# Performance work log

Measured on AMD Instinct MI355X. Metric: run time of the kernel, lower is better.

The kernel has to match this reference:

```python
import jax, jax.numpy as jnp
import numpy as np

B = 16384   # batch (agents x parallel envs)
IN = 12     # input_dim
H = 64      # hidden_dim -> 2H = 128
OUT = 25    # output_dim (forced by x[:,0:5]..x[:,20:25] slicing)


def setup_inputs() -> dict:
    key = jax.random.key(0)
    ks = jax.random.split(key, 24)
    n = lambda k, s: jax.random.normal(k, s, dtype=jnp.float32)
    s = 0.1  # scale params to keep SiLU/softmax in a sane range
    return {
        "x": n(ks[0], (B, IN)),
        "na": 4,
        # mlp_in: Linear(IN, 2H) + SiLU
        "W_in": n(ks[1], (2 * H, IN)) * s, "b_in": n(ks[2], (2 * H,)) * s,
        # first attention (2H)
        "Aq4": n(ks[3], (2 * H, 2 * H)) * s, "Bq4": n(ks[4], (2 * H,)) * s,
        "Ak4": n(ks[5], (2 * H, 2 * H)) * s, "Bk4": n(ks[6], (2 * H,)) * s,
        "Av4": n(ks[7], (2 * H, 2 * H)) * s, "Bv4": n(ks[8], (2 * H,)) * s,
        # mlp_hidden_4: Linear(2H, H) + SiLU
        "W_h": n(ks[9], (H, 2 * H)) * s, "b_h": n(ks[10], (H,)) * s,
        # second attention (H)
        "Aq7": n(ks[11], (H, H)) * s, "Bq7": n(ks[12], (H,)) * s,
        "Ak7": n(ks[13], (H, H)) * s, "Bk7": n(ks[14], (H,)) * s,
        "Av7": n(ks[15], (H, H)) * s, "Bv7": n(ks[16], (H,)) * s,
        # mlp_out: Linear(H, OUT) + SiLU
        "W_out": n(ks[17], (OUT, H)) * s, "b_out": n(ks[18], (OUT,)) * s,
    }


def _attn(h, Aq, Bq, Ak, Bk, Av, Bv):
    # h: [B, D]; torch does bmm(A, x^T)+B with x of shape [B,1,D] -> seq-len-1
    # attention, i.e. scores are an outer product q k^T of shape [B, D, D].
    q = jax.nn.silu(h @ Aq.T + Bq)                      # [B, D]
    k = jax.nn.silu(h @ Ak.T + Bk)                      # [B, D]
    v = jax.nn.silu(h @ Av.T + Bv)                      # [B, D]
    a = jax.nn.softmax(q[:, :, None] * k[:, None, :], axis=2)  # [B, D, D]
    return jax.nn.silu(jnp.einsum("bij,bj->bi", a, v))  # [B, D]


def reference(x, na, W_in, b_in, Aq4, Bq4, Ak4, Bk4, Av4, Bv4,
              W_h, b_h, Aq7, Bq7, Ak7, Bk7, Av7, Bv7, W_out, b_out):
    h = jax.nn.silu(x @ W_in.T + b_in)                  # [B, 2H]
    h = _attn(h, Aq4, Bq4, Ak4, Bk4, Av4, Bv4)          # [B, 2H]
    h = jax.nn.silu(h @ W_h.T + b_h)                    # [B, H]
    h = _attn(h, Aq7, Bq7, Ak7, Bk7, Av7, Bv7)          # [B, H]
    y = jax.nn.silu(h @ W_out.T + b_out)                # [B, 25]

    # block-diagonal quadratic-form assembly (l=2, kron with ones(1,2))
    M11 = jnp.sum(y[:, 0:5] ** 2, axis=1)               # [B]
    M12 = jnp.sum(y[:, 5:10] ** 2, axis=1)
    M21 = jnp.sum(y[:, 10:15] ** 2, axis=1)
    M22 = jnp.sum(y[:, 15:20] ** 2, axis=1)
    Mpp = jnp.sum(y[:, 20:25] ** 2, axis=1)             # [B]
    q = y[:, :4]                                        # [B, 4] = [q0,q1,q2,q3]
    # M = [[diag(M11), diag(M12)],[diag(M21), diag(M22)]] (each 2x2 diag)
    quad = (M11 * (q[:, 0] ** 2 + q[:, 1] ** 2)
            + (M12 + M21) * (q[:, 0] * q[:, 2] + q[:, 1] * q[:, 3])
            + M22 * (q[:, 2] ** 2 + q[:, 3] ** 2))
    return (quad + Mpp)[:, None]                        # [B, 1]
```

## Files before the change

kernel.cpp:

```cpp
#include <hip/hip_runtime.h>

#define RPW 4
#define WAVES 4
#define RPB (RPW * WAVES)
#define NM 14

using short8 = __attribute__((ext_vector_type(8))) short;
using f32x4  = __attribute__((ext_vector_type(4))) float;

#define LOG2E 1.4426950408889634f

static __device__ __forceinline__ float ex2(float x) { return __builtin_amdgcn_exp2f(x); }
static __device__ __forceinline__ float rcpf_(float x) { return __builtin_amdgcn_rcpf(x); }
static __device__ __forceinline__ float silu_(float x) {
    return x * rcpf_(1.0f + ex2(-x * LOG2E));
}
static __device__ __forceinline__ unsigned short bfhi(float x) {
    return (unsigned short)(__float_as_uint(x) >> 16);
}
static __device__ __forceinline__ unsigned short bfrn(float x) {
    unsigned u = __float_as_uint(x);
    return (unsigned short)((u + 0x7fffu + ((u >> 16) & 1u)) >> 16);
}
static __device__ __forceinline__ float bf2f(unsigned short h) {
    return __uint_as_float(((unsigned)h) << 16);
}

template <int CTRL>
static __device__ __forceinline__ float dpp_rot(float v) {
    return __uint_as_float(
        __builtin_amdgcn_update_dpp(0u, __float_as_uint(v), CTRL, 0xF, 0xF, true));
}
static __device__ __forceinline__ float rsum16(float v) {
    v += dpp_rot<0x128>(v);
    v += dpp_rot<0x124>(v);
    v += dpp_rot<0x122>(v);
    v += dpp_rot<0x121>(v);
    return v;
}

__constant__ float c_invfact[15] = {
    1.f, 1.f, 0.5f, 1.f/6, 1.f/24, 1.f/120, 1.f/720, 1.f/5040, 1.f/40320,
    1.f/362880, 1.f/3628800, 1.f/39916800, 1.f/479001600,
    1.f/6227020800.f, 1.f/87178291200.f};

template <int O, int I>
__device__ __forceinline__ void tr(const float* __restrict__ s, float* __restrict__ d,
                                   int t0, int stride) {
    for (int idx = t0; idx < O * I; idx += stride) {
        int o = idx / I, in = idx - o * I;
        d[in * O + o] = s[idx];
    }
}
template <int N>
__device__ __forceinline__ void cvt(const float* __restrict__ s,
                                    unsigned short* __restrict__ hi,
                                    unsigned short* __restrict__ lo,
                                    int t0, int stride) {
    for (int i = t0; i < N; i += stride) {
        float a = s[i];
        unsigned short h = bfhi(a);
        float r = a - bf2f(h);
        hi[i] = h;
        lo[i] = bfhi(r);
    }
}

__global__ void tweights(const float* __restrict__ s0, const float* __restrict__ s1,
                         const float* __restrict__ s2, const float* __restrict__ s3,
                         const float* __restrict__ s4, const float* __restrict__ s5,
                         const float* __restrict__ s6, const float* __restrict__ s7,
                         const float* __restrict__ s8, float* __restrict__ ws) {
    const int stride = gridDim.x * blockDim.x;
    const int t0 = blockIdx.x * blockDim.x + threadIdx.x;
    tr<128, 12>(s0, ws + 0, t0, stride);
    unsigned short* u4 = (unsigned short*)(ws + 1536);
    cvt<128 * 128>(s1, u4 + 0,     u4 + 16384, t0, stride);
    cvt<128 * 128>(s2, u4 + 32768, u4 + 49152, t0, stride);
    cvt<128 * 128>(s3, u4 + 65536, u4 + 81920, t0, stride);
    unsigned short* wh = (unsigned short*)(ws + 50688);
    cvt<64 * 128>(s4, wh + 0, wh + 8192, t0, stride);
    unsigned short* u7 = (unsigned short*)(ws + 58880);
    cvt<64 * 64>(s5, u7 + 0,     u7 + 4096,  t0, stride);
    cvt<64 * 64>(s6, u7 + 8192,  u7 + 12288, t0, stride);
    cvt<64 * 64>(s7, u7 + 16384, u7 + 20480, t0, stride);
    tr<25, 64>(s8, ws + 71168, t0, stride);
}

__global__ __launch_bounds__(256, 4) void fused_net(
    const float* __restrict__ x, const float* __restrict__ ws,
    const float* __restrict__ b_in,
    const float* __restrict__ Bq4, const float* __restrict__ Bk4, const float* __restrict__ Bv4,
    const float* __restrict__ b_h,
    const float* __restrict__ Bq7, const float* __restrict__ Bk7, const float* __restrict__ Bv7,
    const float* __restrict__ b_out,
    float* __restrict__ out) {
    __shared__ __align__(16) unsigned short hAhi[16][136], hAlo[16][136];
    __shared__ __align__(16) unsigned short h2hi[16][80],  h2lo[16][80];
    __shared__ __align__(16) float sQ[16][132];
    __shared__ __align__(16) unsigned short sKVb[16][132][2];
    __shared__ __align__(16) float h3T[WAVES][64][RPW];
    __shared__ __align__(16) float sXT[WAVES][12][RPW];
    __shared__ __align__(16) float sY[WAVES][RPW][26];

    const int tid = threadIdx.x;
    const int w = tid >> 6;
    const int l = tid & 63;
    const int row0 = blockIdx.x * RPB + w * RPW;
    const int m16 = l & 15, quad = l >> 4;
    const int g = l & 15, r = l >> 4;
    const int R = w * RPW + r;

    const float* WinT  = ws + 0;
    const float* WoutT = ws + 71168;

    if (l < 12 * RPW) {
        float v = x[row0 * 12 + l];
        int rr = l / 12, in = l - rr * 12;
        sXT[w][in][rr] = v;
    }

    {
        float2 bb = *(const float2*)&b_in[2 * l];
        float a0[RPW], a1[RPW];
        #pragma unroll
        for (int rr = 0; rr < RPW; rr++) { a0[rr] = bb.x; a1[rr] = bb.y; }
        #pragma unroll
        for (int in = 0; in < 12; in++) {
            float2 wv = *(const float2*)&WinT[in * 128 + 2 * l];
            float4 xr = *(const float4*)&sXT[w][in][0];
            a0[0] = fmaf(xr.x, wv.x, a0[0]); a1[0] = fmaf(xr.x, wv.y, a1[0]);
            a0[1] = fmaf(xr.y, wv.x, a0[1]); a1[1] = fmaf(xr.y, wv.y, a1[1]);
            a0[2] = fmaf(xr.z, wv.x, a0[2]); a1[2] = fmaf(xr.z, wv.y, a1[2]);
            a0[3] = fmaf(xr.w, wv.x, a0[3]); a1[3] = fmaf(xr.w, wv.y, a1[3]);
        }
        #pragma unroll
        for (int rr = 0; rr < RPW; rr++) {
            float h0 = silu_(a0[rr]), h1 = silu_(a1[rr]);
            unsigned short h0h = bfhi(h0), h1h = bfhi(h1);
            float r0 = h0 - bf2f(h0h), r1 = h1 - bf2f(h1h);
            *(unsigned*)&hAhi[w * 4 + rr][2 * l] = (unsigned)h0h | ((unsigned)h1h << 16);
            *(unsigned*)&hAlo[w * 4 + rr][2 * l] = (unsigned)bfhi(r0) | ((unsigned)bfhi(r1) << 16);
        }
    }
    __syncthreads();

    {
        short8 Ah[4], Al[4];
        #pragma unroll
        for (int kt = 0; kt < 4; kt++) {
            Ah[kt] = *(const short8*)&hAhi[m16][kt * 32 + quad * 8];
            Al[kt] = *(const short8*)&hAlo[m16][kt * 32 + quad * 8];
        }
        const unsigned short* u4 = (const unsigned short*)(ws + 1536);
        #pragma unroll
        for (int t = 0; t < 6; t++) {
            const int nt = w * 6 + t;
            const int mat = nt >> 3;
            const int n = (nt & 7) * 16 + m16;
            const float* bp = (mat == 0) ? Bq4 : (mat == 1) ? Bk4 : Bv4;
            float b = bp[n];
            f32x4 acc = {b, b, b, b};
            const unsigned short* Bh = u4 + mat * 32768 + n * 128;
            const unsigned short* Bl = Bh + 16384;
            #pragma unroll
            for (int kt = 0; kt < 4; kt++) {
                short8 bh = *(const short8*)&Bh[kt * 32 + quad * 8];
                short8 bl = *(const short8*)&Bl[kt * 32 + quad * 8];
                acc = __builtin_amdgcn_mfma_f32_16x16x32_bf16(Ah[kt], bh, acc, 0, 0, 0);
                acc = __builtin_amdgcn_mfma_f32_16x16x32_bf16(Ah[kt], bl, acc, 0, 0, 0);
                acc = __builtin_amdgcn_mfma_f32_16x16x32_bf16(Al[kt], bh, acc, 0, 0, 0);
            }
            #pragma unroll
            for (int reg = 0; reg < 4; reg++) {
                int row = quad * 4 + reg;
                float val = silu_(acc[reg]);
                if (mat == 0)      sQ[row][n] = val;
                else if (mat == 1) sKVb[row][n][0] = bfrn(val);
                else               sKVb[row][n][1] = bfrn(val);
            }
        }
    }
    __syncthreads();

    {
        float dmom[NM];
        float nmom[NM + 1];
        #pragma unroll
        for (int m = 0; m < NM; m++) dmom[m] = 0.f;
        #pragma unroll
        for (int m = 0; m <= NM; m++) nmom[m] = 0.f;
        uint4 u0 = *(const uint4*)&sKVb[R][g * 8][0];
        uint4 u1 = *(const uint4*)&sKVb[R][g * 8 + 4][0];
        unsigned us[8] = {u0.x, u0.y, u0.z, u0.w, u1.x, u1.y, u1.z, u1.w};
        #pragma unroll
        for (int jj = 0; jj < 8; jj++) {
            unsigned u = us[jj];
            float kf = __uint_as_float(u << 16);
            float vf = __uint_as_float(u & 0xffff0000u);
            nmom[0] += vf;
            float p = kf;
            dmom[0] += p; nmom[1] = fmaf(vf, p, nmom[1]);
            #pragma unroll
            for (int m = 1; m < NM; m++) {
                p *= kf;
                dmom[m] += p;
                nmom[m + 1] = fmaf(vf, p, nmom[m + 1]);
            }
        }
        #pragma unroll
        for (int m = 0; m < NM; m++) dmom[m] = rsum16(dmom[m]);
        #pragma unroll
        for (int m = 0; m <= NM; m++) nmom[m] = rsum16(nmom[m]);
        float cd[NM + 1], cn[NM + 1];
        cd[0] = 128.f; cn[0] = nmom[0];
        #pragma unroll
        for (int m = 1; m <= NM; m++) {
            cd[m] = dmom[m - 1] * c_invfact[m];
            cn[m] = nmom[m] * c_invfact[m];
        }
        float4 qa = *(const float4*)&sQ[R][g * 8];
        float4 qb = *(const float4*)&sQ[R][g * 8 + 4];
        float qs[8] = {qa.x, qa.y, qa.z, qa.w, qb.x, qb.y, qb.z, qb.w};
        unsigned hiw[4], low[4];
        #pragma unroll
        for (int i = 0; i < 8; i++) {
            float t = qs[i];
            float d = cd[NM], nn = cn[NM];
            #pragma unroll
            for (int m = NM - 1; m >= 0; m--) {
                d = fmaf(d, t, cd[m]);
                nn = fmaf(nn, t, cn[m]);
            }
            float o = silu_(nn * rcpf_(d));
            unsigned short oh = bfhi(o);
            unsigned short olo = bfhi(o - bf2f(oh));
            if (i & 1) { hiw[i >> 1] |= ((unsigned)oh) << 16; low[i >> 1] |= ((unsigned)olo) << 16; }
            else       { hiw[i >> 1] = oh; low[i >> 1] = olo; }
        }
        *(uint4*)&hAhi[R][g * 8] = make_uint4(hiw[0], hiw[1], hiw[2], hiw[3]);
        *(uint4*)&hAlo[R][g * 8] = make_uint4(low[0], low[1], low[2], low[3]);
    }
    __syncthreads();

    {
        short8 Ah[4], Al[4];
        #pragma unroll
        for (int kt = 0; kt < 4; kt++) {
            Ah[kt] = *(const short8*)&hAhi[m16][kt * 32 + quad * 8];
            Al[kt] = *(const short8*)&hAlo[m16][kt * 32 + quad * 8];
        }
        const unsigned short* whh = (const unsigned short*)(ws + 50688);
        const unsigned short* whl = whh + 8192;
        const int n = w * 16 + m16;
        float b = b_h[n];
        f32x4 acc = {b, b, b, b};
        #pragma unroll
        for (int kt = 0; kt < 4; kt++) {
            short8 bh = *(const short8*)&whh[n * 128 + kt * 32 + quad * 8];
            short8 bl = *(const short8*)&whl[n * 128 + kt * 32 + quad * 8];
            acc = __builtin_amdgcn_mfma_f32_16x16x32_bf16(Ah[kt], bh, acc, 0, 0, 0);
            acc = __builtin_amdgcn_mfma_f32_16x16x32_bf16(Ah[kt], bl, acc, 0, 0, 0);
            acc = __builtin_amdgcn_mfma_f32_16x16x32_bf16(Al[kt], bh, acc, 0, 0, 0);
        }
        #pragma unroll
        for (int reg = 0; reg < 4; reg++) {
            int row = quad * 4 + reg;
            float hv = silu_(acc[reg]);
            unsigned short hh = bfhi(hv);
            h2hi[row][n] = hh;
            h2lo[row][n] = bfhi(hv - bf2f(hh));
        }
    }
    __syncthreads();

    {
        short8 Ah[2], Al[2];
        #pragma unroll
        for (int kt = 0; kt < 2; kt++) {
            Ah[kt] = *(const short8*)&h2hi[m16][kt * 32 + quad * 8];
            Al[kt] = *(const short8*)&h2lo[m16][kt * 32 + quad * 8];
        }
        const unsigned short* u7 = (const unsigned short*)(ws + 58880);
        #pragma unroll
        for (int t = 0; t < 3; t++) {
            const int nt = w * 3 + t;
            const int mat = nt >> 2;
            const int n = (nt & 3) * 16 + m16;
            const float* bp = (mat == 0) ? Bq7 : (mat == 1) ? Bk7 : Bv7;
            float b = bp[n];
            f32x4 acc = {b, b, b, b};
            const unsigned short* Bh = u7 + mat * 8192 + n * 64;
            const unsigned short* Bl = Bh + 4096;
            #pragma unroll
            for (int kt = 0; kt < 2; kt++) {
                short8 bh = *(const short8*)&Bh[kt * 32 + quad * 8];
                short8 bl = *(const short8*)&Bl[kt * 32 + quad * 8];
                acc = __builtin_amdgcn_mfma_f32_16x16x32_bf16(Ah[kt], bh, acc, 0, 0, 0);
                acc = __builtin_amdgcn_mfma_f32_16x16x32_bf16(Ah[kt], bl, acc, 0, 0, 0);
                acc = __builtin_amdgcn_mfma_f32_16x16x32_bf16(Al[kt], bh, acc, 0, 0, 0);
            }
            #pragma unroll
            for (int reg = 0; reg < 4; reg++) {
                int row = quad * 4 + reg;
                float val = silu_(acc[reg]);
                if (mat == 0)      sQ[row][n] = val;
                else if (mat == 1) sKVb[row][n][0] = bfrn(val);
                else               sKVb[row][n][1] = bfrn(val);
            }
        }
    }
    __syncthreads();

    {
        float dmom[NM];
        float nmom[NM + 1];
        #pragma unroll
        for (int m = 0; m < NM; m++) dmom[m] = 0.f;
        #pragma unroll
        for (int m = 0; m <= NM; m++) nmom[m] = 0.f;
        uint4 u0 = *(const uint4*)&sKVb[R][g * 4][0];
        unsigned us[4] = {u0.x, u0.y, u0.z, u0.w};
        #pragma unroll
        for (int jj = 0; jj < 4; jj++) {
            unsigned u = us[jj];
            float kf = __uint_as_float(u << 16);
            float vf = __uint_as_float(u & 0xffff0000u);
            nmom[0] += vf;
            float p = kf;
            dmom[0] += p; nmom[1] = fmaf(vf, p, nmom[1]);
            #pragma unroll
            for (int m = 1; m < NM; m++) {
                p *= kf;
                dmom[m] += p;
                nmom[m + 1] = fmaf(vf, p, nmom[m + 1]);
            }
        }
        #pragma unroll
        for (int m = 0; m < NM; m++) dmom[m] = rsum16(dmom[m]);
        #pragma unroll
        for (int m = 0; m <= NM; m++) nmom[m] = rsum16(nmom[m]);
        float cd[NM + 1], cn[NM + 1];
        cd[0] = 64.f; cn[0] = nmom[0];
        #pragma unroll
        for (int m = 1; m <= NM; m++) {
            cd[m] = dmom[m - 1] * c_invfact[m];
            cn[m] = nmom[m] * c_invfact[m];
        }
        float4 qa = *(const float4*)&sQ[R][g * 4];
        float qs[4] = {qa.x, qa.y, qa.z, qa.w};
        #pragma unroll
        for (int i = 0; i < 4; i++) {
            float t = qs[i];
            float d = cd[NM], nn = cn[NM];
            #pragma unroll
            for (int m = NM - 1; m >= 0; m--) {
                d = fmaf(d, t, cd[m]);
                nn = fmaf(nn, t, cn[m]);
            }
            h3T[w][g * 4 + i][r] = silu_(nn * rcpf_(d));
        }
    }

    {
        const int o = l & 31;
        const int half = l >> 5;
        const int oc = (o < 25) ? o : 0;
        float y[RPW];
        float bb = (half == 0) ? b_out[oc] : 0.f;
        #pragma unroll
        for (int rr = 0; rr < RPW; rr++) y[rr] = bb;
        const int in0 = half * 32;
        #pragma unroll 4
        for (int i = 0; i < 32; i++) {
            int in = in0 + i;
            float wv = WoutT[in * 25 + oc];
            float4 xr = *(const float4*)&h3T[w][in][0];
            y[0] = fmaf(xr.x, wv, y[0]);
            y[1] = fmaf(xr.y, wv, y[1]);
            y[2] = fmaf(xr.z, wv, y[2]);
            y[3] = fmaf(xr.w, wv, y[3]);
        }
        #pragma unroll
        for (int rr = 0; rr < RPW; rr++) {
            float full = y[rr] + __shfl_xor(y[rr], 32, 64);
            if (l < 25) sY[w][rr][l] = silu_(full);
        }
    }

    if (l < RPW) {
        const int rr = l;
        float y[25];
        #pragma unroll
        for (int c = 0; c < 25; c++) y[c] = sY[w][rr][c];
        float M11 = 0.f, M12 = 0.f, M21 = 0.f, M22 = 0.f, Mpp = 0.f;
        #pragma unroll
        for (int c = 0; c < 5; c++) {
            M11 = fmaf(y[c], y[c], M11);
            M12 = fmaf(y[5 + c], y[5 + c], M12);
            M21 = fmaf(y[10 + c], y[10 + c], M21);
            M22 = fmaf(y[15 + c], y[15 + c], M22);
            Mpp = fmaf(y[20 + c], y[20 + c], Mpp);
        }
        float quad = M11 * (y[0] * y[0] + y[1] * y[1])
                   + (M12 + M21) * (y[0] * y[2] + y[1] * y[3])
                   + M22 * (y[2] * y[2] + y[3] * y[3]);
        out[row0 + rr] = quad + Mpp;
    }
}

extern "C" void kernel_launch(void* const* d_in, const int* in_sizes, int n_in,
                              void* d_out, int out_size, void* d_ws, size_t ws_size,
                              hipStream_t stream) {
    const float* x    = (const float*)d_in[0];
    const float* W_in = (const float*)d_in[2];
    const float* b_in = (const float*)d_in[3];
    const float* Aq4  = (const float*)d_in[4];
    const float* Bq4  = (const float*)d_in[5];
    const float* Ak4  = (const float*)d_in[6];
    const float* Bk4  = (const float*)d_in[7];
    const float* Av4  = (const float*)d_in[8];
    const float* Bv4  = (const float*)d_in[9];
    const float* W_h  = (const float*)d_in[10];
    const float* b_h  = (const float*)d_in[11];
    const float* Aq7  = (const float*)d_in[12];
    const float* Bq7  = (const float*)d_in[13];
    const float* Ak7  = (const float*)d_in[14];
    const float* Bk7  = (const float*)d_in[15];
    const float* Av7  = (const float*)d_in[16];
    const float* Bv7  = (const float*)d_in[17];
    const float* Wout = (const float*)d_in[18];
    const float* bout = (const float*)d_in[19];
    float* ws = (float*)d_ws;

    tweights<<<256, 256, 0, stream>>>(W_in, Aq4, Ak4, Av4, W_h, Aq7, Ak7, Av7, Wout, ws);

    const int B = in_sizes[0] / 12;
    const int grid = B / RPB;
    fused_net<<<grid, 256, 0, stream>>>(x, ws, b_in, Bq4, Bk4, Bv4,
                                        b_h, Bq7, Bk7, Bv7, bout, (float*)d_out);
}
```

Before: 137.1 us.

## Halve rows per wave and spread attention moments across 32 lanes

Reduces rows per wave from 4 to 2 (8 rows per block), so each row's attention moment computation is spread over 32 lanes instead of 16. Each lane now handles half as many keys and queries, and a ds_swizzle step extends the DPP reduction to 32 lanes. MFMA tiles still compute 16 rows but only the first 8 are valid, which wastes half of the matrix-core work, and the grid doubles in size. Launch bounds are raised to 8 blocks per CU to gain occupancy, at the risk of register pressure.

```diff
diff --git a/kernel.cpp b/kernel.cpp
--- a/kernel.cpp
+++ b/kernel.cpp
@@ -1,6 +1,6 @@
 #include <hip/hip_runtime.h>
 
-#define RPW 4
+#define RPW 2
 #define WAVES 4
 #define RPB (RPW * WAVES)
 #define NM 14
@@ -36,6 +36,12 @@
     v += dpp_rot<0x124>(v);
     v += dpp_rot<0x122>(v);
     v += dpp_rot<0x121>(v);
+    return v;
+}
+static __device__ __forceinline__ float rsum32(float v) {
+    v = rsum16(v);
+    v += __uint_as_float(
+        (unsigned)__builtin_amdgcn_ds_swizzle((int)__float_as_uint(v), 0x401F));
     return v;
 }
 
@@ -87,7 +93,7 @@
     tr<25, 64>(s8, ws + 71168, t0, stride);
 }
 
-__global__ __launch_bounds__(256, 4) void fused_net(
+__global__ __launch_bounds__(256, 8) void fused_net(
     const float* __restrict__ x, const float* __restrict__ ws,
     const float* __restrict__ b_in,
     const float* __restrict__ Bq4, const float* __restrict__ Bk4, const float* __restrict__ Bv4,
@@ -95,10 +101,10 @@
     const float* __restrict__ Bq7, const float* __restrict__ Bk7, const float* __restrict__ Bv7,
     const float* __restrict__ b_out,
     float* __restrict__ out) {
-    __shared__ __align__(16) unsigned short hAhi[16][136], hAlo[16][136];
-    __shared__ __align__(16) unsigned short h2hi[16][80],  h2lo[16][80];
-    __shared__ __align__(16) float sQ[16][132];
-    __shared__ __align__(16) unsigned short sKVb[16][132][2];
+    __shared__ __align__(16) unsigned short hAhi[8][136], hAlo[8][136];
+    __shared__ __align__(16) unsigned short h2hi[8][80],  h2lo[8][80];
+    __shared__ __align__(16) float sQ[8][132];
+    __shared__ __align__(16) unsigned short sKVb[8][132][2];
     __shared__ __align__(16) float h3T[WAVES][64][RPW];
     __shared__ __align__(16) float sXT[WAVES][12][RPW];
     __shared__ __align__(16) float sY[WAVES][RPW][26];
@@ -108,7 +114,8 @@
     const int l = tid & 63;
     const int row0 = blockIdx.x * RPB + w * RPW;
     const int m16 = l & 15, quad = l >> 4;
-    const int g = l & 15, r = l >> 4;
+    const int m8 = m16 & 7;
+    const int g = l & 31, r = l >> 5;
     const int R = w * RPW + r;
 
     const float* WinT  = ws + 0;
@@ -128,19 +135,17 @@
         #pragma unroll
         for (int in = 0; in < 12; in++) {
             float2 wv = *(const float2*)&WinT[in * 128 + 2 * l];
-            float4 xr = *(const float4*)&sXT[w][in][0];
+            float2 xr = *(const float2*)&sXT[w][in][0];
             a0[0] = fmaf(xr.x, wv.x, a0[0]); a1[0] = fmaf(xr.x, wv.y, a1[0]);
             a0[1] = fmaf(xr.y, wv.x, a0[1]); a1[1] = fmaf(xr.y, wv.y, a1[1]);
-            a0[2] = fmaf(xr.z, wv.x, a0[2]); a1[2] = fmaf(xr.z, wv.y, a1[2]);
-            a0[3] = fmaf(xr.w, wv.x, a0[3]); a1[3] = fmaf(xr.w, wv.y, a1[3]);
         }
         #pragma unroll
         for (int rr = 0; rr < RPW; rr++) {
             float h0 = silu_(a0[rr]), h1 = silu_(a1[rr]);
             unsigned short h0h = bfhi(h0), h1h = bfhi(h1);
             float r0 = h0 - bf2f(h0h), r1 = h1 - bf2f(h1h);
-            *(unsigned*)&hAhi[w * 4 + rr][2 * l] = (unsigned)h0h | ((unsigned)h1h << 16);
-            *(unsigned*)&hAlo[w * 4 + rr][2 * l] = (unsigned)bfhi(r0) | ((unsigned)bfhi(r1) << 16);
+            *(unsigned*)&hAhi[w * RPW + rr][2 * l] = (unsigned)h0h | ((unsigned)h1h << 16);
+            *(unsigned*)&hAlo[w * RPW + rr][2 * l] = (unsigned)bfhi(r0) | ((unsigned)bfhi(r1) << 16);
         }
     }
     __syncthreads();
@@ -149,8 +154,8 @@
         short8 Ah[4], Al[4];
         #pragma unroll
         for (int kt = 0; kt < 4; kt++) {
-            Ah[kt] = *(const short8*)&hAhi[m16][kt * 32 + quad * 8];
-            Al[kt] = *(const short8*)&hAlo[m16][kt * 32 + quad * 8];
+            Ah[kt] = *(const short8*)&hAhi[m8][kt * 32 + quad * 8];
+            Al[kt] = *(const short8*)&hAlo[m8][kt * 32 + quad * 8];
         }
         const unsigned short* u4 = (const unsigned short*)(ws + 1536);
         #pragma unroll
@@ -171,13 +176,15 @@
                 acc = __builtin_amdgcn_mfma_f32_16x16x32_bf16(Ah[kt], bl, acc, 0, 0, 0);
                 acc = __builtin_amdgcn_mfma_f32_16x16x32_bf16(Al[kt], bh, acc, 0, 0, 0);
             }
-            #pragma unroll
-            for (int reg = 0; reg < 4; reg++) {
-                int row = quad * 4 + reg;
-                float val = silu_(acc[reg]);
-                if (mat == 0)      sQ[row][n] = val;
-                else if (mat == 1) sKVb[row][n][0] = bfrn(val);
-                else               sKVb[row][n][1] = bfrn(val);
+            if (quad < 2) {
+                #pragma unroll
+                for (int reg = 0; reg < 4; reg++) {
+                    int row = quad * 4 + reg;
+                    float val = silu_(acc[reg]);
+                    if (mat == 0)      sQ[row][n] = val;
+                    else if (mat == 1) sKVb[row][n][0] = bfrn(val);
+                    else               sKVb[row][n][1] = bfrn(val);
+                }
             }
         }
     }
@@ -190,11 +197,10 @@
         for (int m = 0; m < NM; m++) dmom[m] = 0.f;
         #pragma unroll
         for (int m = 0; m <= NM; m++) nmom[m] = 0.f;
-        uint4 u0 = *(const uint4*)&sKVb[R][g * 8][0];
-        uint4 u1 = *(const uint4*)&sKVb[R][g * 8 + 4][0];
-        unsigned us[8] = {u0.x, u0.y, u0.z, u0.w, u1.x, u1.y, u1.z, u1.w};
-        #pragma unroll
-        for (int jj = 0; jj < 8; jj++) {
+        uint4 u0 = *(const uint4*)&sKVb[R][g * 4][0];
+        unsigned us[4] = {u0.x, u0.y, u0.z, u0.w};
+        #pragma unroll
+        for (int jj = 0; jj < 4; jj++) {
             unsigned u = us[jj];
             float kf = __uint_as_float(u << 16);
             float vf = __uint_as_float(u & 0xffff0000u);
@@ -209,9 +215,9 @@
             }
         }
         #pragma unroll
-        for (int m = 0; m < NM; m++) dmom[m] = rsum16(dmom[m]);
-        #pragma unroll
-        for (int m = 0; m <= NM; m++) nmom[m] = rsum16(nmom[m]);
+        for (int m = 0; m < NM; m++) dmom[m] = rsum32(dmom[m]);
+        #pragma unroll
+        for (int m = 0; m <= NM; m++) nmom[m] = rsum32(nmom[m]);
         float cd[NM + 1], cn[NM + 1];
         cd[0] = 128.f; cn[0] = nmom[0];
         #pragma unroll
@@ -219,12 +225,11 @@
             cd[m] = dmom[m - 1] * c_invfact[m];
             cn[m] = nmom[m] * c_invfact[m];
         }
-        float4 qa = *(const float4*)&sQ[R][g * 8];
-        float4 qb = *(const float4*)&sQ[R][g * 8 + 4];
-        float qs[8] = {qa.x, qa.y, qa.z, qa.w, qb.x, qb.y, qb.z, qb.w};
-        unsigned hiw[4], low[4];
-        #pragma unroll
-        for (int i = 0; i < 8; i++) {
+        float4 qa = *(const float4*)&sQ[R][g * 4];
+        float qs[4] = {qa.x, qa.y, qa.z, qa.w};
+        unsigned hiw[2], low[2];
+        #pragma unroll
+        for (int i = 0; i < 4; i++) {
             float t = qs[i];
             float d = cd[NM], nn = cn[NM];
             #pragma unroll
@@ -238,8 +243,8 @@
             if (i & 1) { hiw[i >> 1] |= ((unsigned)oh) << 16; low[i >> 1] |= ((unsigned)olo) << 16; }
             else       { hiw[i >> 1] = oh; low[i >> 1] = olo; }
         }
-        *(uint4*)&hAhi[R][g * 8] = make_uint4(hiw[0], hiw[1], hiw[2], hiw[3]);
-        *(uint4*)&hAlo[R][g * 8] = make_uint4(low[0], low[1], low[2], low[3]);
+        *(uint2*)&hAhi[R][g * 4] = make_uint2(hiw[0], hiw[1]);
+        *(uint2*)&hAlo[R][g * 4] = make_uint2(low[0], low[1]);
     }
     __syncthreads();
 
@@ -247,8 +252,8 @@
         short8 Ah[4], Al[4];
         #pragma unroll
         for (int kt = 0; kt < 4; kt++) {
-            Ah[kt] = *(const short8*)&hAhi[m16][kt * 32 + quad * 8];
-            Al[kt] = *(const short8*)&hAlo[m16][kt * 32 + quad * 8];
+            Ah[kt] = *(const short8*)&hAhi[m8][kt * 32 + quad * 8];
+            Al[kt] = *(const short8*)&hAlo[m8][kt * 32 + quad * 8];
         }
         const unsigned short* whh = (const unsigned short*)(ws + 50688);
         const unsigned short* whl = whh + 8192;
@@ -263,13 +268,15 @@
             acc = __builtin_amdgcn_mfma_f32_16x16x32_bf16(Ah[kt], bl, acc, 0, 0, 0);
             acc = __builtin_amdgcn_mfma_f32_16x16x32_bf16(Al[kt], bh, acc, 0, 0, 0);
         }
-        #pragma unroll
-        for (int reg = 0; reg < 4; reg++) {
-            int row = quad * 4 + reg;
-            float hv = silu_(acc[reg]);
-            unsigned short hh = bfhi(hv);
-            h2hi[row][n] = hh;
-            h2lo[row][n] = bfhi(hv - bf2f(hh));
+        if (quad < 2) {
+            #pragma unroll
+            for (int reg = 0; reg < 4; reg++) {
+                int row = quad * 4 + reg;
+                float hv = silu_(acc[reg]);
+                unsigned short hh = bfhi(hv);
+                h2hi[row][n] = hh;
+                h2lo[row][n] = bfhi(hv - bf2f(hh));
+            }
         }
     }
     __syncthreads();
@@ -278,8 +285,8 @@
         short8 Ah[2], Al[2];
         #pragma unroll
         for (int kt = 0; kt < 2; kt++) {
-            Ah[kt] = *(const short8*)&h2hi[m16][kt * 32 + quad * 8];
-            Al[kt] = *(const short8*)&h2lo[m16][kt * 32 + quad * 8];
+            Ah[kt] = *(const short8*)&h2hi[m8][kt * 32 + quad * 8];
+            Al[kt] = *(const short8*)&h2lo[m8][kt * 32 + quad * 8];
         }
         const unsigned short* u7 = (const unsigned short*)(ws + 58880);
         #pragma unroll
@@ -300,13 +307,15 @@
                 acc = __builtin_amdgcn_mfma_f32_16x16x32_bf16(Ah[kt], bl, acc, 0, 0, 0);
                 acc = __builtin_amdgcn_mfma_f32_16x16x32_bf16(Al[kt], bh, acc, 0, 0, 0);
             }
-            #pragma unroll
-            for (int reg = 0; reg < 4; reg++) {
-                int row = quad * 4 + reg;
-                float val = silu_(acc[reg]);
-                if (mat == 0)      sQ[row][n] = val;
-                else if (mat == 1) sKVb[row][n][0] = bfrn(val);
-                else               sKVb[row][n][1] = bfrn(val);
+            if (quad < 2) {
+                #pragma unroll
+                for (int reg = 0; reg < 4; reg++) {
+                    int row = quad * 4 + reg;
+                    float val = silu_(acc[reg]);
+                    if (mat == 0)      sQ[row][n] = val;
+                    else if (mat == 1) sKVb[row][n][0] = bfrn(val);
+                    else               sKVb[row][n][1] = bfrn(val);
+                }
             }
         }
     }
@@ -319,10 +328,10 @@
         for (int m = 0; m < NM; m++) dmom[m] = 0.f;
         #pragma unroll
         for (int m = 0; m <= NM; m++) nmom[m] = 0.f;
-        uint4 u0 = *(const uint4*)&sKVb[R][g * 4][0];
-        unsigned us[4] = {u0.x, u0.y, u0.z, u0.w};
-        #pragma unroll
-        for (int jj = 0; jj < 4; jj++) {
+        uint2 u0 = *(const uint2*)&sKVb[R][g * 2][0];
+        unsigned us[2] = {u0.x, u0.y};
+        #pragma unroll
+        for (int jj = 0; jj < 2; jj++) {
             unsigned u = us[jj];
             float kf = __uint_as_float(u << 16);
             float vf = __uint_as_float(u & 0xffff0000u);
@@ -337,9 +346,9 @@
             }
         }
         #pragma unroll
-        for (int m = 0; m < NM; m++) dmom[m] = rsum16(dmom[m]);
-        #pragma unroll
-        for (int m = 0; m <= NM; m++) nmom[m] = rsum16(nmom[m]);
+        for (int m = 0; m < NM; m++) dmom[m] = rsum32(dmom[m]);
+        #pragma unroll
+        for (int m = 0; m <= NM; m++) nmom[m] = rsum32(nmom[m]);
         float cd[NM + 1], cn[NM + 1];
         cd[0] = 64.f; cn[0] = nmom[0];
         #pragma unroll
@@ -347,10 +356,10 @@
             cd[m] = dmom[m - 1] * c_invfact[m];
             cn[m] = nmom[m] * c_invfact[m];
         }
-        float4 qa = *(const float4*)&sQ[R][g * 4];
-        float qs[4] = {qa.x, qa.y, qa.z, qa.w};
-        #pragma unroll
-        for (int i = 0; i < 4; i++) {
+        float2 qa = *(const float2*)&sQ[R][g * 2];
+        float qs[2] = {qa.x, qa.y};
+        #pragma unroll
+        for (int i = 0; i < 2; i++) {
             float t = qs[i];
             float d = cd[NM], nn = cn[NM];
             #pragma unroll
@@ -358,7 +367,7 @@
                 d = fmaf(d, t, cd[m]);
                 nn = fmaf(nn, t, cn[m]);
             }
-            h3T[w][g * 4 + i][r] = silu_(nn * rcpf_(d));
+            h3T[w][g * 2 + i][r] = silu_(nn * rcpf_(d));
         }
     }
 
@@ -375,11 +384,9 @@
         for (int i = 0; i < 32; i++) {
             int in = in0 + i;
             float wv = WoutT[in * 25 + oc];
-            float4 xr = *(const float4*)&h3T[w][in][0];
+            float2 xr = *(const float2*)&h3T[w][in][0];
             y[0] = fmaf(xr.x, wv, y[0]);
             y[1] = fmaf(xr.y, wv, y[1]);
-            y[2] = fmaf(xr.z, wv, y[2]);
-            y[3] = fmaf(xr.w, wv, y[3]);
         }
         #pragma unroll
         for (int rr = 0; rr < RPW; rr++) {
```

Result: slower. 173.7 us (+26.7%).

## Drop weight preprocessing kernel; split weights to bf16 hi/lo inside fused kernel

Applied to the files above, without the earlier changes.

Removes the separate tweights launch that transposed weights and pre-split them into bf16 hi/lo planes in a workspace. The fused kernel now reads the original fp32 weights directly and splits them in registers with a new cvt8 helper before each MFMA. W_in and W_out are read in their native row-major layout with vector loads instead of from transposed copies. This saves a kernel launch and a pass over the weights, but every block repeats the conversion arithmetic and loads twice as many bytes of fp32 weights per tile.

```diff
diff --git a/kernel.cpp b/kernel.cpp
--- a/kernel.cpp
+++ b/kernel.cpp
@@ -24,6 +24,27 @@
 }
 static __device__ __forceinline__ float bf2f(unsigned short h) {
     return __uint_as_float(((unsigned)h) << 16);
+}
+
+static __device__ __forceinline__ void cvt8(const float* __restrict__ p,
+                                            short8& hi, short8& lo) {
+    float4 a = *(const float4*)p;
+    float4 b = *(const float4*)(p + 4);
+    float v[8] = {a.x, a.y, a.z, a.w, b.x, b.y, b.z, b.w};
+    unsigned hw[4], lw[4];
+    #pragma unroll
+    for (int i = 0; i < 4; i++) {
+        unsigned u0 = __float_as_uint(v[2 * i]);
+        unsigned u1 = __float_as_uint(v[2 * i + 1]);
+        hw[i] = (u0 >> 16) | (u1 & 0xffff0000u);
+        float r0 = v[2 * i]     - __uint_as_float(u0 & 0xffff0000u);
+        float r1 = v[2 * i + 1] - __uint_as_float(u1 & 0xffff0000u);
+        lw[i] = (__float_as_uint(r0) >> 16) | (__float_as_uint(r1) & 0xffff0000u);
+    }
+    uint4 hu = make_uint4(hw[0], hw[1], hw[2], hw[3]);
+    uint4 lu = make_uint4(lw[0], lw[1], lw[2], lw[3]);
+    hi = __builtin_bit_cast(short8, hu);
+    lo = __builtin_bit_cast(short8, lu);
 }
 
 template <int CTRL>
@@ -44,56 +65,17 @@
     1.f/362880, 1.f/3628800, 1.f/39916800, 1.f/479001600,
     1.f/6227020800.f, 1.f/87178291200.f};
 
-template <int O, int I>
-__device__ __forceinline__ void tr(const float* __restrict__ s, float* __restrict__ d,
-                                   int t0, int stride) {
-    for (int idx = t0; idx < O * I; idx += stride) {
-        int o = idx / I, in = idx - o * I;
-        d[in * O + o] = s[idx];
-    }
-}
-template <int N>
-__device__ __forceinline__ void cvt(const float* __restrict__ s,
-                                    unsigned short* __restrict__ hi,
-                                    unsigned short* __restrict__ lo,
-                                    int t0, int stride) {
-    for (int i = t0; i < N; i += stride) {
-        float a = s[i];
-        unsigned short h = bfhi(a);
-        float r = a - bf2f(h);
-        hi[i] = h;
-        lo[i] = bfhi(r);
-    }
-}
-
-__global__ void tweights(const float* __restrict__ s0, const float* __restrict__ s1,
-                         const float* __restrict__ s2, const float* __restrict__ s3,
-                         const float* __restrict__ s4, const float* __restrict__ s5,
-                         const float* __restrict__ s6, const float* __restrict__ s7,
-                         const float* __restrict__ s8, float* __restrict__ ws) {
-    const int stride = gridDim.x * blockDim.x;
-    const int t0 = blockIdx.x * blockDim.x + threadIdx.x;
-    tr<128, 12>(s0, ws + 0, t0, stride);
-    unsigned short* u4 = (unsigned short*)(ws + 1536);
-    cvt<128 * 128>(s1, u4 + 0,     u4 + 16384, t0, stride);
-    cvt<128 * 128>(s2, u4 + 32768, u4 + 49152, t0, stride);
-    cvt<128 * 128>(s3, u4 + 65536, u4 + 81920, t0, stride);
-    unsigned short* wh = (unsigned short*)(ws + 50688);
-    cvt<64 * 128>(s4, wh + 0, wh + 8192, t0, stride);
-    unsigned short* u7 = (unsigned short*)(ws + 58880);
-    cvt<64 * 64>(s5, u7 + 0,     u7 + 4096,  t0, stride);
-    cvt<64 * 64>(s6, u7 + 8192,  u7 + 12288, t0, stride);
-    cvt<64 * 64>(s7, u7 + 16384, u7 + 20480, t0, stride);
-    tr<25, 64>(s8, ws + 71168, t0, stride);
-}
-
 __global__ __launch_bounds__(256, 4) void fused_net(
-    const float* __restrict__ x, const float* __restrict__ ws,
-    const float* __restrict__ b_in,
-    const float* __restrict__ Bq4, const float* __restrict__ Bk4, const float* __restrict__ Bv4,
-    const float* __restrict__ b_h,
-    const float* __restrict__ Bq7, const float* __restrict__ Bk7, const float* __restrict__ Bv7,
-    const float* __restrict__ b_out,
+    const float* __restrict__ x,
+    const float* __restrict__ W_in, const float* __restrict__ b_in,
+    const float* __restrict__ Aq4, const float* __restrict__ Bq4,
+    const float* __restrict__ Ak4, const float* __restrict__ Bk4,
+    const float* __restrict__ Av4, const float* __restrict__ Bv4,
+    const float* __restrict__ W_h, const float* __restrict__ b_h,
+    const float* __restrict__ Aq7, const float* __restrict__ Bq7,
+    const float* __restrict__ Ak7, const float* __restrict__ Bk7,
+    const float* __restrict__ Av7, const float* __restrict__ Bv7,
+    const float* __restrict__ Wout, const float* __restrict__ b_out,
     float* __restrict__ out) {
     __shared__ __align__(16) unsigned short hAhi[16][136], hAlo[16][136];
     __shared__ __align__(16) unsigned short h2hi[16][80],  h2lo[16][80];
@@ -111,9 +93,6 @@
     const int g = l & 15, r = l >> 4;
     const int R = w * RPW + r;
 
-    const float* WinT  = ws + 0;
-    const float* WoutT = ws + 71168;
-
     if (l < 12 * RPW) {
         float v = x[row0 * 12 + l];
         int rr = l / 12, in = l - rr * 12;
@@ -121,18 +100,25 @@
     }
 
     {
+        float wr0[12], wr1[12];
+        const float* w0p = W_in + (2 * l) * 12;
+        const float* w1p = W_in + (2 * l + 1) * 12;
+        #pragma unroll
+        for (int q = 0; q < 3; q++) {
+            *(float4*)&wr0[4 * q] = *(const float4*)&w0p[4 * q];
+            *(float4*)&wr1[4 * q] = *(const float4*)&w1p[4 * q];
+        }
         float2 bb = *(const float2*)&b_in[2 * l];
         float a0[RPW], a1[RPW];
         #pragma unroll
         for (int rr = 0; rr < RPW; rr++) { a0[rr] = bb.x; a1[rr] = bb.y; }
         #pragma unroll
         for (int in = 0; in < 12; in++) {
-            float2 wv = *(const float2*)&WinT[in * 128 + 2 * l];
             float4 xr = *(const float4*)&sXT[w][in][0];
-            a0[0] = fmaf(xr.x, wv.x, a0[0]); a1[0] = fmaf(xr.x, wv.y, a1[0]);
-            a0[1] = fmaf(xr.y, wv.x, a0[1]); a1[1] = fmaf(xr.y, wv.y, a1[1]);
-            a0[2] = fmaf(xr.z, wv.x, a0[2]); a1[2] = fmaf(xr.z, wv.y, a1[2]);
-            a0[3] = fmaf(xr.w, wv.x, a0[3]); a1[3] = fmaf(xr.w, wv.y, a1[3]);
+            a0[0] = fmaf(xr.x, wr0[in], a0[0]); a1[0] = fmaf(xr.x, wr1[in], a1[0]);
+            a0[1] = fmaf(xr.y, wr0[in], a0[1]); a1[1] = fmaf(xr.y, wr1[in], a1[1]);
+            a0[2] = fmaf(xr.z, wr0[in], a0[2]); a1[2] = fmaf(xr.z, wr1[in], a1[2]);
+            a0[3] = fmaf(xr.w, wr0[in], a0[3]); a1[3] = fmaf(xr.w, wr1[in], a1[3]);
         }
         #pragma unroll
         for (int rr = 0; rr < RPW; rr++) {
@@ -152,21 +138,20 @@
             Ah[kt] = *(const short8*)&hAhi[m16][kt * 32 + quad * 8];
             Al[kt] = *(const short8*)&hAlo[m16][kt * 32 + quad * 8];
         }
-        const unsigned short* u4 = (const unsigned short*)(ws + 1536);
         #pragma unroll
         for (int t = 0; t < 6; t++) {
             const int nt = w * 6 + t;
             const int mat = nt >> 3;
             const int n = (nt & 7) * 16 + m16;
+            const float* Ap = (mat == 0) ? Aq4 : (mat == 1) ? Ak4 : Av4;
             const float* bp = (mat == 0) ? Bq4 : (mat == 1) ? Bk4 : Bv4;
             float b = bp[n];
             f32x4 acc = {b, b, b, b};
-            const unsigned short* Bh = u4 + mat * 32768 + n * 128;
-            const unsigned short* Bl = Bh + 16384;
+            const float* Bp = Ap + n * 128 + quad * 8;
             #pragma unroll
             for (int kt = 0; kt < 4; kt++) {
-                short8 bh = *(const short8*)&Bh[kt * 32 + quad * 8];
-                short8 bl = *(const short8*)&Bl[kt * 32 + quad * 8];
+                short8 bh, bl;
+                cvt8(Bp + kt * 32, bh, bl);
                 acc = __builtin_amdgcn_mfma_f32_16x16x32_bf16(Ah[kt], bh, acc, 0, 0, 0);
                 acc = __builtin_amdgcn_mfma_f32_16x16x32_bf16(Ah[kt], bl, acc, 0, 0, 0);
                 acc = __builtin_amdgcn_mfma_f32_16x16x32_bf16(Al[kt], bh, acc, 0, 0, 0);
@@ -250,15 +235,14 @@
             Ah[kt] = *(const short8*)&hAhi[m16][kt * 32 + quad * 8];
             Al[kt] = *(const short8*)&hAlo[m16][kt * 32 + quad * 8];
         }
-        const unsigned short* whh = (const unsigned short*)(ws + 50688);
-        const unsigned short* whl = whh + 8192;
         const int n = w * 16 + m16;
         float b = b_h[n];
         f32x4 acc = {b, b, b, b};
+        const float* Bp = W_h + n * 128 + quad * 8;
         #pragma unroll
         for (int kt = 0; kt < 4; kt++) {
-            short8 bh = *(const short8*)&whh[n * 128 + kt * 32 + quad * 8];
-            short8 bl = *(const short8*)&whl[n * 128 + kt * 32 + quad * 8];
+            short8 bh, bl;
+            cvt8(Bp + kt * 32, bh, bl);
             acc = __builtin_amdgcn_mfma_f32_16x16x32_bf16(Ah[kt], bh, acc, 0, 0, 0);
             acc = __builtin_amdgcn_mfma_f32_16x16x32_bf16(Ah[kt], bl, acc, 0, 0, 0);
             acc = __builtin_amdgcn_mfma_f32_16x16x32_bf16(Al[kt], bh, acc, 0, 0, 0);
@@ -281,21 +265,20 @@
             Ah[kt] = *(const short8*)&h2hi[m16][kt * 32 + quad * 8];
             Al[kt] = *(const short8*)&h2lo[m16][kt * 32 + quad * 8];
         }
-        const unsigned short* u7 = (const unsigned short*)(ws + 58880);
         #pragma unroll
         for (int t = 0; t < 3; t++) {
             const int nt = w * 3 + t;
             const int mat = nt >> 2;
             const int n = (nt & 3) * 16 + m16;
+            const float* Ap = (mat == 0) ? Aq7 : (mat == 1) ? Ak7 : Av7;
             const float* bp = (mat == 0) ? Bq7 : (mat == 1) ? Bk7 : Bv7;
             float b = bp[n];
             f32x4 acc = {b, b, b, b};
-            const unsigned short* Bh = u7 + mat * 8192 + n * 64;
-            const unsigned short* Bl = Bh + 4096;
+            const float* Bp = Ap + n * 64 + quad * 8;
             #pragma unroll
             for (int kt = 0; kt < 2; kt++) {
-                short8 bh = *(const short8*)&Bh[kt * 32 + quad * 8];
-                short8 bl = *(const short8*)&Bl[kt * 32 + quad * 8];
+                short8 bh, bl;
+                cvt8(Bp + kt * 32, bh, bl);
                 acc = __builtin_amdgcn_mfma_f32_16x16x32_bf16(Ah[kt], bh, acc, 0, 0, 0);
                 acc = __builtin_amdgcn_mfma_f32_16x16x32_bf16(Ah[kt], bl, acc, 0, 0, 0);
                 acc = __builtin_amdgcn_mfma_f32_16x16x32_bf16(Al[kt], bh, acc, 0, 0, 0);
@@ -319,8 +302,9 @@
         for (int m = 0; m < NM; m++) dmom[m] = 0.f;
         #pragma unroll
         for (int m = 0; m <= NM; m++) nmom[m] = 0.f;
-        uint4 u0 = *(const uint4*)&sKVb[R][g * 4][0];
-        unsigned us[4] = {u0.x, u0.y, u0.z, u0.w};
+        uint2 u0 = *(const uint2*)&sKVb[R][g * 4][0];
+        uint2 u1 = *(const uint2*)&sKVb[R][g * 4 + 2][0];
+        unsigned us[4] = {u0.x, u0.y, u1.x, u1.y};
         #pragma unroll
         for (int jj = 0; jj < 4; jj++) {
             unsigned u = us[jj];
@@ -371,15 +355,20 @@
         #pragma unroll
         for (int rr = 0; rr < RPW; rr++) y[rr] = bb;
         const int in0 = half * 32;
-        #pragma unroll 4
-        for (int i = 0; i < 32; i++) {
-            int in = in0 + i;
-            float wv = WoutT[in * 25 + oc];
-            float4 xr = *(const float4*)&h3T[w][in][0];
-            y[0] = fmaf(xr.x, wv, y[0]);
-            y[1] = fmaf(xr.y, wv, y[1]);
-            y[2] = fmaf(xr.z, wv, y[2]);
-            y[3] = fmaf(xr.w, wv, y[3]);
+        const float* wp = Wout + oc * 64 + in0;
+        #pragma unroll
+        for (int q = 0; q < 8; q++) {
+            float4 wq = *(const float4*)&wp[4 * q];
+            float wa[4] = {wq.x, wq.y, wq.z, wq.w};
+            #pragma unroll
+            for (int ii = 0; ii < 4; ii++) {
+                int in = in0 + 4 * q + ii;
+                float4 xr = *(const float4*)&h3T[w][in][0];
+                y[0] = fmaf(xr.x, wa[ii], y[0]);
+                y[1] = fmaf(xr.y, wa[ii], y[1]);
+                y[2] = fmaf(xr.z, wa[ii], y[2]);
+                y[3] = fmaf(xr.w, wa[ii], y[3]);
+            }
         }
         #pragma unroll
         for (int rr = 0; rr < RPW; rr++) {
@@ -431,12 +420,13 @@
     const float* Bv7  = (const float*)d_in[17];
     const float* Wout = (const float*)d_in[18];
     const float* bout = (const float*)d_in[19];
-    float* ws = (float*)d_ws;
-
-    tweights<<<256, 256, 0, stream>>>(W_in, Aq4, Ak4, Av4, W_h, Aq7, Ak7, Av7, Wout, ws);
+    (void)d_ws; (void)ws_size;
 
     const int B = in_sizes[0] / 12;
     const int grid = B / RPB;
-    fused_net<<<grid, 256, 0, stream>>>(x, ws, b_in, Bq4, Bk4, Bv4,
-                                        b_h, Bq7, Bk7, Bv7, bout, (float*)d_out);
-}
+    fused_net<<<grid, 256, 0, stream>>>(x, W_in, b_in,
+                                        Aq4, Bq4, Ak4, Bk4, Av4, Bv4,
+                                        W_h, b_h,
+                                        Aq7, Bq7, Ak7, Bk7, Av7, Bv7,
+                                        Wout, bout, (float*)d_out);
+}
```

Result: slower. 150.7 us (+9.9%).
